# Kernel optimization log

Hardware: AMD Instinct MI355X
Metric: run time of the kernel (lower is better)

The kernel has to match this reference:

```python
import jax, jax.numpy as jnp
import numpy as np

ALPHA = 0.9
T = 809          # doc_len_limit hard-coded in fofe_tricontext_encoder
M = 16           # opt['max_len'] (cand_len_limit)
BN_EPS = 1e-5


def _cand_indices(T, M):
    # Enumeration order matches get_sample_index: outer over start s, inner over span.
    s_list, e_list = [], []
    for s in range(T):
        for span in range(min(M, T - s)):
            s_list.append(s)
            e_list.append(s + span)
    return np.asarray(s_list, np.int32), np.asarray(e_list, np.int32)

_S_IDX, _E_IDX = _cand_indices(T, M)          # [N_CANDS] = [12824]
_SPAN = (_E_IDX - _S_IDX).astype(np.int64)
# FOFE decay coefficient alpha^(e-s+1) for subtracting the prefix before the span
_COEF = (ALPHA ** (_SPAN + 1)).astype(np.float32)
# Lower-triangular FOFE prefix operator: A[t,k] = alpha^(t-k) for k<=t
_DIFF = np.subtract.outer(np.arange(T), np.arange(T))
_AFWD = np.where(_DIFF >= 0, ALPHA ** np.maximum(_DIFF, 0), 0.0).astype(np.float32)


def _bn(x, g, b, m, v):
    return (x - m) * jax.lax.rsqrt(v + BN_EPS) * g + b


def _forward(doc_emb, query_emb, W1, g1, b1, m1, v1, W2, g2, b2, m2, v2, W3):
    B, Tt, Dd = doc_emb.shape
    A = jnp.asarray(_AFWD)
    # forward FOFE prefixes F[t] = sum_{k<=t} alpha^(t-k) x[k]; inverse FOFE suffixes
    F = jnp.einsum('tk,bkd->btd', A, doc_emb)          # [B,T,Dd]
    R = jnp.einsum('tk,bkd->btd', A.T, doc_emb)        # [B,T,Dd]
    Fp = jnp.concatenate([jnp.zeros((B, 1, Dd), F.dtype), F], axis=1)   # Fp[:,s]=F[s-1]
    Rp = jnp.concatenate([R, jnp.zeros((B, 1, Dd), R.dtype)], axis=1)   # Rp[:,e+1]
    s_idx = jnp.asarray(_S_IDX)
    e_idx = jnp.asarray(_E_IDX)
    coef = jnp.asarray(_COEF)
    lctx = Fp[:, s_idx]                                 # left context excl cand
    cand = F[:, e_idx] - coef[None, :, None] * Fp[:, s_idx]  # FOFE of span [s,e]
    rctx = Rp[:, e_idx + 1]                             # right context excl cand
    doc_fofe = jnp.concatenate([lctx, cand, rctx], axis=-1)  # [B,N,3*Dd]
    # query FOFE (fofe_linear): z = sum_t alpha^(Lq-1-t) q[t]
    Lq = query_emb.shape[1]
    w = (ALPHA ** jnp.arange(Lq - 1, -1, -1, dtype=jnp.float32))
    qf = jnp.einsum('t,btd->bd', w, query_emb)          # [B,E]
    N = doc_fofe.shape[1]
    qf_b = jnp.broadcast_to(qf[:, None, :], (B, N, qf.shape[-1]))
    dq = jnp.concatenate([doc_fofe, qf_b], axis=-1)     # [B,N,3*Dd+E]
    x = dq.reshape(B * N, -1)
    h = jax.nn.relu(_bn(x @ W1.T, g1, b1, m1, v1))      # 1x1 conv == GEMM
    h = jax.nn.relu(_bn(h @ W2.T, g2, b2, m2, v2))
    out = (h @ W3.T).reshape(B, N, 2)                   # 2 class scores per candidate
    return out


def setup_inputs() -> dict:
    key = jax.random.key(0)
    ks = jax.random.split(key, 13)
    B, Lq, Dd, E = 4, 30, 304, 300
    Cin, H4, H2 = 3 * Dd + E, 1024, 512
    return {
        'doc_emb': jax.random.normal(ks[0], (B, T, Dd), jnp.float32),
        'query_emb': jax.random.normal(ks[1], (B, Lq, E), jnp.float32),
        'W1': jax.random.normal(ks[2], (H4, Cin), jnp.float32) / np.sqrt(Cin),
        'g1': jax.random.normal(ks[3], (H4,), jnp.float32),
        'b1': jax.random.normal(ks[4], (H4,), jnp.float32),
        'm1': jax.random.normal(ks[5], (H4,), jnp.float32),
        'v1': jax.random.uniform(ks[6], (H4,), jnp.float32),
        'W2': jax.random.normal(ks[7], (H2, H4), jnp.float32) / np.sqrt(H4),
        'g2': jax.random.normal(ks[8], (H2,), jnp.float32),
        'b2': jax.random.normal(ks[9], (H2,), jnp.float32),
        'm2': jax.random.normal(ks[10], (H2,), jnp.float32),
        'v2': jax.random.uniform(ks[11], (H2,), jnp.float32),
        'W3': jax.random.normal(ks[12], (2, H2), jnp.float32) / np.sqrt(H2),
    }


def reference(doc_emb, query_emb, W1, g1, b1, m1, v1, W2, g2, b2, m2, v2, W3):
    return _forward(doc_emb, query_emb, W1, g1, b1, m1, v1, W2, g2, b2, m2, v2, W3)
```

## Files before the change

kernel.cpp:

```cpp
#include <hip/hip_runtime.h>
#include <string.h>

#define T_LEN   809
#define DD      304
#define EE      300
#define LQ      30
#define NCAND   12824
#define NPAD    12928
#define CIN     1212
#define H1      1024
#define H2      512
#define BATCH   4
#define MROWS_F (BATCH * NPAD)
#define KS      320
#define TPAD    3328
#define NROWS_U 3240

#define MP_SCAN0   0
#define MP_W1      416
#define MP_W2      4256
#define MP_BIAS2   6304
#define MP_BASE    6306
#define MP_RMAP    7330
#define MP_TOTAL   7532

__device__ __constant__ float c_coef[16] = {
  0.9f, 0.81f, 0.729f, 0.6561f, 0.59049f, 0.531441f, 0.4782969f, 0.43046721f,
  0.387420489f, 0.3486784401f, 0.31381059609f, 0.282429536481f,
  0.2541865828329f, 0.22876792454961f, 0.205891132094649f, 0.1853020188851841f
};

__device__ __forceinline__ unsigned short f2bf(float f) {
  unsigned int u = __float_as_uint(f);
  u += 0x7fffu + ((u >> 16) & 1u);
  return (unsigned short)(u >> 16);
}
__device__ __forceinline__ float bf2f(unsigned int h) {
  return __uint_as_float(h << 16);
}

typedef const __attribute__((address_space(1))) unsigned int GU32;
typedef __attribute__((address_space(3))) unsigned int LU32;
__device__ __forceinline__ void async16(const unsigned short* g, unsigned short* l) {
  __builtin_amdgcn_global_load_lds((GU32*)g, (LU32*)l, 16, 0, 0);
}

__device__ __forceinline__ unsigned int comb2(unsigned int ul, unsigned int uc,
                                              unsigned int ue, float cf) {
  float xlo = bf2f(ul & 0xffff) + bf2f(ue & 0xffff) - cf * bf2f(uc & 0xffff);
  float xhi = bf2f(ul >> 16)    + bf2f(ue >> 16)    - cf * bf2f(uc >> 16);
  xlo = xlo > 0.f ? xlo : 0.f;
  xhi = xhi > 0.f ? xhi : 0.f;
  return (unsigned int)f2bf(xlo) | ((unsigned int)f2bf(xhi) << 16);
}
__device__ __forceinline__ unsigned int add2(unsigned int a, unsigned int b) {
  const float lo = bf2f(a & 0xffff) + bf2f(b & 0xffff);
  const float hi = bf2f(a >> 16)    + bf2f(b >> 16);
  return (unsigned int)f2bf(lo) | ((unsigned int)f2bf(hi) << 16);
}

__global__ __launch_bounds__(256) void k_prep(const float* __restrict__ doc,
                                              const float* __restrict__ qe,
                                              const float* __restrict__ W1,
                                              const float* __restrict__ g1,
                                              const float* __restrict__ b1,
                                              const float* __restrict__ m1,
                                              const float* __restrict__ v1,
                                              const float* __restrict__ W2,
                                              const float* __restrict__ g2,
                                              const float* __restrict__ b2,
                                              const float* __restrict__ m2,
                                              const float* __restrict__ v2,
                                              unsigned short* __restrict__ Fz,
                                              unsigned short* __restrict__ Rz,
                                              unsigned short* __restrict__ Wlc,
                                              unsigned short* __restrict__ Wr,
                                              unsigned short* __restrict__ W2b,
                                              float* __restrict__ bias2,
                                              float* __restrict__ baseW,
                                              unsigned int* __restrict__ rowmap)
{
  __shared__ float qs[EE];
  const int vb  = blockIdx.x;
  const int tid = threadIdx.x;

  if (vb < MP_W1) {
    const int dchunk = vb & 1;
    const int rest   = vb >> 1;
    const int tchunk = rest % 26;
    const int b      = (rest / 26) & 3;
    const int dir    = rest / 104;
    const int d  = dchunk * 256 + tid;
    const int t0 = tchunk * 32;
    if (dir == 0) {
      if (tchunk == 0 && d < KS) Fz[((size_t)b * 810) * KS + d] = 0;
      if (d >= DD) return;
      const float* db = doc + (size_t)b * T_LEN * DD + d;
      int start = t0 - 96; if (start < 0) start = 0;
      int end = t0 + 31; if (end > T_LEN - 1) end = T_LEN - 1;
      float s = 0.f;
      for (int t = start; t <= end; ++t) {
        s = fmaf(0.9f, s, db[(size_t)t * DD]);
        if (t >= t0) Fz[((size_t)b * 810 + 1 + t) * KS + d] = f2bf(s);
      }
    } else {
      if (tchunk == 0 && d < KS) Rz[((size_t)b * 810 + 809) * KS + d] = 0;
      if (d >= DD) return;
      const float* db = doc + (size_t)b * T_LEN * DD + d;
      int t1 = t0 + 31; if (t1 > T_LEN - 1) t1 = T_LEN - 1;
      int start = t1 + 96; if (start > T_LEN - 1) start = T_LEN - 1;
      float s = 0.f;
      for (int t = start; t >= t0; --t) {
        s = fmaf(0.9f, s, db[(size_t)t * DD]);
        if (t <= t1) Rz[((size_t)b * 810 + t) * KS + d] = f2bf(s);
      }
    }
  } else if (vb < MP_W2) {
    const int e = (vb - MP_W1) * 256 + tid;
    const int j = e / KS;
    const int k = e - j * KS;
    int jj, koff; unsigned short* dst; size_t idx;
    if (j < 1024)      { jj = j;        koff = k;       dst = Wlc; idx = (size_t)j * KS + k; }
    else if (j < 2048) { jj = j - 1024; koff = 304 + k; dst = Wlc; idx = (size_t)j * KS + k; }
    else               { jj = j - 2048; koff = 608 + k; dst = Wr;  idx = (size_t)(j - 2048) * KS + k; }
    float w = 0.f;
    if (k < 304) w = W1[(size_t)jj * CIN + koff] * g1[jj] * rsqrtf(v1[jj] + 1e-5f);
    dst[idx] = f2bf(w);
  } else if (vb < MP_BIAS2) {
    const int e = (vb - MP_W2) * 256 + tid;
    const int j = e >> 10;
    const int k = e & 1023;
    const float w = W2[(size_t)j * H1 + k] * g2[j] * rsqrtf(v2[j] + 1e-5f);
    W2b[(size_t)j * H1 + k] = f2bf(w);
  } else if (vb < MP_BASE) {
    const int i = (vb - MP_BIAS2) * 256 + tid;
    if (i < H2) {
      const float s = g2[i] * rsqrtf(v2[i] + 1e-5f);
      bias2[i] = b2[i] - m2[i] * s;
    }
  } else if (vb < MP_RMAP) {
    const int flat = vb - MP_BASE;
    const int b  = flat >> 8;
    const int jg = flat & 255;
    const float* q = qe + (size_t)b * LQ * EE;
    for (int k = tid; k < EE; k += 256) {
      float s = 0.f;
      for (int t = 0; t < LQ; ++t) s = fmaf(s, 0.9f, q[(size_t)t * EE + k]);
      qs[k] = s;
    }
    __syncthreads();
    const int wv   = tid >> 6;
    const int lane = tid & 63;
    const int j = jg * 4 + wv;
    const float* w = W1 + (size_t)j * CIN + 912;
    float acc = 0.f;
    for (int k = lane; k < EE; k += 64) acc = fmaf(qs[k], w[k], acc);
    #pragma unroll
    for (int off = 32; off; off >>= 1) acc += __shfl_down(acc, off);
    if (lane == 0) {
      const float sc = g1[j] * rsqrtf(v1[j] + 1e-5f);
      baseW[(size_t)b * 2048 + j]        = b1[j] - m1[j] * sc + acc * sc;
      baseW[(size_t)b * 2048 + 1024 + j] = 0.f;
    }
  } else {
    const int g = (vb - MP_RMAP) * 256 + tid;
    const int b  = g / NPAD;
    const int rr = g - b * NPAD;
    unsigned int mv = 0;
    if (rr < NCAND) {
      int s, span;
      if (rr < 12704) { s = rr >> 4; span = rr & 15; }
      else {
        const int x = rr - 12704;
        int d = 0;
        while (d < 14 && x >= (15 * (d + 1) - ((d + 1) * d) / 2)) ++d;
        span = x - (15 * d - (d * (d - 1)) / 2);
        s = 794 + d;
      }
      const unsigned int srow = (unsigned int)(b * 810 + s);
      const unsigned int erow = (unsigned int)(b * 810 + s + span + 1);
      mv = srow | (erow << 12) | ((unsigned int)span << 24);
    }
    rowmap[g] = mv;
  }
}

typedef __attribute__((ext_vector_type(8))) short frag8;
typedef __attribute__((ext_vector_type(4))) float f32x4;

#define GEMM_KLOOP(A_, B_, K_)                                                   \
  __shared__ __align__(16) unsigned short As[128 * 32];                          \
  __shared__ __align__(16) unsigned short Bs[128 * 32];                          \
  const int tid  = threadIdx.x;                                                  \
  const int lane = tid & 63;                                                     \
  const int wv   = tid >> 6;                                                     \
  const int wm   = wv & 1, wn = wv >> 1;                                         \
  const int lr = lane >> 2;                                                      \
  const int lc = lane & 3;                                                       \
  const int sc = lc ^ ((lr >> 1) & 3);                                           \
  const unsigned short* gA = A_ + ((size_t)bm * 128 + wv * 32 + lr) * K_ + sc * 8; \
  const unsigned short* gB = B_ + ((size_t)bn * 128 + wv * 32 + lr) * K_ + sc * 8; \
  const size_t row16 = (size_t)16 * K_;                                          \
  unsigned short* lA0 = &As[wv * 1024];                                          \
  unsigned short* lB0 = &Bs[wv * 1024];                                          \
  f32x4 acc[4][4];                                                               \
  _Pragma("unroll")                                                              \
  for (int i = 0; i < 4; ++i)                                                    \
    _Pragma("unroll")                                                            \
    for (int j = 0; j < 4; ++j) acc[i][j] = (f32x4){0.f, 0.f, 0.f, 0.f};         \
  const int arow = lane & 15;                                                    \
  const int pg   = (lane >> 4) ^ ((arow >> 1) & 3);                              \
  const int aoff = (wm * 64 + arow) * 32 + pg * 8;                               \
  const int boff = (wn * 64 + arow) * 32 + pg * 8;                               \
  for (int kc = 0; kc < K_; kc += 32) {                                          \
    __syncthreads();                                                             \
    async16(gA + kc,         lA0);                                               \
    async16(gA + kc + row16, lA0 + 512);                                         \
    async16(gB + kc,         lB0);                                               \
    async16(gB + kc + row16, lB0 + 512);                                         \
    __syncthreads();                                                             \
    frag8 a[4], b[4];                                                            \
    _Pragma("unroll")                                                            \
    for (int i = 0; i < 4; ++i) a[i] = *(const frag8*)&As[aoff + i * 512];       \
    _Pragma("unroll")                                                            \
    for (int i = 0; i < 4; ++i) b[i] = *(const frag8*)&Bs[boff + i * 512];       \
    _Pragma("unroll")                                                            \
    for (int i = 0; i < 4; ++i)                                                  \
      _Pragma("unroll")                                                          \
      for (int j = 0; j < 4; ++j)                                                \
        acc[i][j] = __builtin_amdgcn_mfma_f32_16x16x32_bf16(a[i], b[j], acc[i][j], 0, 0, 0); \
  }

__global__ __launch_bounds__(256, 4) void k_ugemm(const unsigned short* __restrict__ Fz,
                                                  const unsigned short* __restrict__ Wlc,
                                                  const unsigned short* __restrict__ Rz,
                                                  const unsigned short* __restrict__ Wr,
                                                  const float* __restrict__ baseW,
                                                  unsigned short* __restrict__ UF,
                                                  unsigned short* __restrict__ UR)
{
  int bx = blockIdx.x;
  const int isUF = (bx < 416);
  const unsigned short *Ap, *Bp; unsigned short* Cp; int bn, bm, Nout;
  if (isUF) { Ap = Fz; Bp = Wlc; Cp = UF; bn = bx & 15; bm = bx >> 4; Nout = 2048; }
  else { bx -= 416; Ap = Rz; Bp = Wr; Cp = UR; bn = bx & 7; bm = bx >> 3; Nout = 1024; }
  GEMM_KLOOP(Ap, Bp, KS)
  const int crow0 = bm * 128 + wm * 64 + ((lane >> 4) << 2);
  const int ccol0 = bn * 128 + wn * 64 + arow;
  #pragma unroll
  for (int i = 0; i < 4; ++i)
    #pragma unroll
    for (int j = 0; j < 4; ++j) {
      const int col = ccol0 + j * 16;
      #pragma unroll
      for (int r = 0; r < 4; ++r) {
        const int row = crow0 + i * 16 + r;
        float v = acc[i][j][r];
        if (isUF) {
          int bb = row / 810; if (bb > 3) bb = 3;
          v += baseW[(size_t)bb * 2048 + col];
        }
        Cp[(size_t)row * Nout + col] = f2bf(v);
      }
    }
}

__global__ __launch_bounds__(256) void k_ucr(const unsigned short* __restrict__ UF,
                                             const unsigned short* __restrict__ UR,
                                             unsigned short* __restrict__ UCR)
{
  const int c = blockIdx.x * 256 + threadIdx.x;
  if (c >= NROWS_U * 128) return;
  const int t  = c >> 7;
  const int kk = (c & 127) * 8;
  const uint4 a = *(const uint4*)(UF + (size_t)t * 2048 + 1024 + kk);
  const uint4 b = *(const uint4*)(UR + (size_t)t * 1024 + kk);
  uint4 o;
  o.x = add2(a.x, b.x);
  o.y = add2(a.y, b.y);
  o.z = add2(a.z, b.z);
  o.w = add2(a.w, b.w);
  *(uint4*)(UCR + (size_t)t * 1024 + kk) = o;
}

__global__ __launch_bounds__(512, 2) void k_gemm2f(const unsigned short* __restrict__ UF,
                                                   const unsigned short* __restrict__ UCR,
                                                   const unsigned short* __restrict__ W2b,
                                                   const unsigned int* __restrict__ rowmap,
                                                   const float* __restrict__ bias,
                                                   const float* __restrict__ W3,
                                                   float* __restrict__ out)
{
  __shared__ __align__(16) unsigned short As[128 * 32];
  __shared__ __align__(16) unsigned short Bs[512 * 32];

  const int orig = blockIdx.x;
  const int xcd = orig & 7, cidx = orig >> 3;
  const int bm = (xcd < 4 ? xcd * 51 : 204 + (xcd - 4) * 50) + cidx;

  const int tid  = threadIdx.x;
  const int lane = tid & 63;
  const int w    = tid >> 6;
  const int wm   = w & 1;
  const int wn   = w >> 1;
  const int arow = lane & 15;
  const int lr   = lane >> 2;
  const int lc   = lane & 3;
  const int sc   = lc ^ ((lr >> 1) & 3);

  const int rA    = tid >> 2;
  const int cA    = tid & 3;
  const int physA = cA ^ ((rA >> 1) & 3);
  const unsigned int mv = rowmap[bm * 128 + rA];
  const float cf = c_coef[mv >> 24];
  const unsigned short* pUL = UF  + (size_t)(mv & 4095) * 2048 + cA * 8;
  const unsigned short* pUE = UCR + (size_t)((mv >> 12) & 4095) * 1024 + cA * 8;
  unsigned short* wAd = &As[rA * 32 + physA * 8];

  const unsigned short* gB = W2b + ((size_t)(w * 64 + lr)) * H1 + sc * 8;
  unsigned short* lB = &Bs[w * 2048];

  const int pg   = (lane >> 4) ^ ((arow >> 1) & 3);
  const int aoff = (wm * 64 + arow) * 32 + pg * 8;
  const int boff = (wn * 128 + arow) * 32 + pg * 8;

  f32x4 acc[4][8];
  #pragma unroll
  for (int i = 0; i < 4; ++i)
    #pragma unroll
    for (int j = 0; j < 8; ++j) acc[i][j] = (f32x4){0.f, 0.f, 0.f, 0.f};

  uint4 vul = *(const uint4*)(pUL);
  uint4 vuc = *(const uint4*)(pUL + 1024);
  uint4 vue = *(const uint4*)(pUE);

  for (int kc = 0; kc < H1; kc += 32) {
    __syncthreads();
    async16(gB + kc,            lB);
    async16(gB + kc + 16 * H1,  lB + 512);
    async16(gB + kc + 32 * H1,  lB + 1024);
    async16(gB + kc + 48 * H1,  lB + 1536);
    {
      uint4 o;
      o.x = comb2(vul.x, vuc.x, vue.x, cf);
      o.y = comb2(vul.y, vuc.y, vue.y, cf);
      o.z = comb2(vul.z, vuc.z, vue.z, cf);
      o.w = comb2(vul.w, vuc.w, vue.w, cf);
      *(uint4*)wAd = o;
    }
    const int kn = kc + 32;
    if (kn < H1) {
      vul = *(const uint4*)(pUL + kn);
      vuc = *(const uint4*)(pUL + 1024 + kn);
      vue = *(const uint4*)(pUE + kn);
      __builtin_amdgcn_sched_barrier(0);
      asm volatile("s_waitcnt vmcnt(3) lgkmcnt(0)" ::: "memory");
    } else {
      __builtin_amdgcn_sched_barrier(0);
      asm volatile("s_waitcnt vmcnt(0) lgkmcnt(0)" ::: "memory");
    }
    __builtin_amdgcn_s_barrier();
    __builtin_amdgcn_sched_barrier(0);

    frag8 a[4], b[8];
    #pragma unroll
    for (int i = 0; i < 4; ++i) a[i] = *(const frag8*)&As[aoff + i * 512];
    #pragma unroll
    for (int j = 0; j < 8; ++j) b[j] = *(const frag8*)&Bs[boff + j * 512];
    #pragma unroll
    for (int i = 0; i < 4; ++i)
      #pragma unroll
      for (int j = 0; j < 8; ++j)
        acc[i][j] = __builtin_amdgcn_mfma_f32_16x16x32_bf16(a[i], b[j], acc[i][j], 0, 0, 0);
  }

  __syncthreads();
  float* redf = (float*)As;

  float bj[8], w0v[8], w1v[8];
  #pragma unroll
  for (int j = 0; j < 8; ++j) {
    const int col = wn * 128 + j * 16 + arow;
    bj[j]  = bias[col];
    w0v[j] = W3[col];
    w1v[j] = W3[H2 + col];
  }
  const int grp = lane >> 4;
  #pragma unroll
  for (int i = 0; i < 4; ++i)
    #pragma unroll
    for (int r = 0; r < 4; ++r) {
      float q0 = 0.f, q1 = 0.f;
      #pragma unroll
      for (int j = 0; j < 8; ++j) {
        float v = acc[i][j][r] + bj[j];
        v = v > 0.f ? v : 0.f;
        q0 = fmaf(v, w0v[j], q0);
        q1 = fmaf(v, w1v[j], q1);
      }
      #pragma unroll
      for (int m = 1; m < 16; m <<= 1) { q0 += __shfl_xor(q0, m); q1 += __shfl_xor(q1, m); }
      if (arow == 0) {
        const int rl = wm * 64 + i * 16 + grp * 4 + r;
        redf[rl * 8 + wn * 2 + 0] = q0;
        redf[rl * 8 + wn * 2 + 1] = q1;
      }
    }
  __syncthreads();
  if (tid < 256) {
    const int rl = tid >> 1, s = tid & 1;
    const float v = redf[rl * 8 + 0 + s] + redf[rl * 8 + 2 + s]
                  + redf[rl * 8 + 4 + s] + redf[rl * 8 + 6 + s];
    const int row = bm * 128 + rl;
    const int b   = row / NPAD;
    const int rr  = row - b * NPAD;
    if (rr < NCAND) out[((size_t)b * NCAND + rr) * 2 + s] = v;
  }
}

extern "C" void kernel_launch(void* const* d_in, const int* in_sizes, int n_in,
                              void* d_out, int out_size, void* d_ws, size_t ws_size,
                              hipStream_t stream)
{
  const float* doc = (const float*)d_in[0];
  const float* qe  = (const float*)d_in[1];
  const float* W1  = (const float*)d_in[2];
  const float* g1  = (const float*)d_in[3];
  const float* b1  = (const float*)d_in[4];
  const float* m1  = (const float*)d_in[5];
  const float* v1  = (const float*)d_in[6];
  const float* W2  = (const float*)d_in[7];
  const float* g2  = (const float*)d_in[8];
  const float* b2  = (const float*)d_in[9];
  const float* m2  = (const float*)d_in[10];
  const float* v2  = (const float*)d_in[11];
  const float* W3  = (const float*)d_in[12];
  float* out = (float*)d_out;

  char* ws = (char*)d_ws;
  size_t off = 0;
  auto alloc = [&](size_t bytes) -> void* {
    void* p = ws + off;
    off = (off + bytes + 255) & ~(size_t)255;
    return p;
  };
  unsigned short* Fz    = (unsigned short*)alloc((size_t)TPAD * KS * 2);
  unsigned short* Rz    = (unsigned short*)alloc((size_t)TPAD * KS * 2);
  unsigned short* Wlc   = (unsigned short*)alloc((size_t)2048 * KS * 2);
  unsigned short* Wr    = (unsigned short*)alloc((size_t)1024 * KS * 2);
  unsigned short* W2b   = (unsigned short*)alloc((size_t)H2 * H1 * 2);
  float*          bias2 = (float*)alloc((size_t)H2 * 4);
  float*          baseW = (float*)alloc((size_t)BATCH * 2048 * 4);
  unsigned short* UF    = (unsigned short*)alloc((size_t)TPAD * 2048 * 2);
  unsigned short* UR    = (unsigned short*)alloc((size_t)TPAD * 1024 * 2);
  unsigned short* UCR   = (unsigned short*)alloc((size_t)NROWS_U * 1024 * 2);
  unsigned int*   rowmap= (unsigned int*)alloc((size_t)MROWS_F * 4);
  (void)ws_size;

  k_prep<<<dim3(MP_TOTAL), 256, 0, stream>>>(doc, qe, W1, g1, b1, m1, v1,
                                             W2, g2, b2, m2, v2,
                                             Fz, Rz, Wlc, Wr, W2b, bias2, baseW, rowmap);
  k_ugemm<<<dim3(416 + 208), 256, 0, stream>>>(Fz, Wlc, Rz, Wr, baseW, UF, UR);
  k_ucr<<<dim3((NROWS_U * 128 + 255) / 256), 256, 0, stream>>>(UF, UR, UCR);
  k_gemm2f<<<dim3(404), 512, 0, stream>>>(UF, UCR, W2b, rowmap, bias2, W3, out);
}
```

Measured before the change: 240.9 us.

## Double-buffer LDS tiles in fused second GEMM and raise MFMA priority

Result: faster. 234.1 us (-2.8%).

```diff
diff --git a/kernel.cpp b/kernel.cpp
--- a/kernel.cpp
+++ b/kernel.cpp
@@ -291,8 +291,8 @@
                                                    const float* __restrict__ W3,
                                                    float* __restrict__ out)
 {
-  __shared__ __align__(16) unsigned short As[128 * 32];
-  __shared__ __align__(16) unsigned short Bs[512 * 32];
+  __shared__ __align__(16) unsigned short As[2 * 128 * 32];
+  __shared__ __align__(16) unsigned short Bs[2 * 512 * 32];
 
   const int orig = blockIdx.x;
   const int xcd = orig & 7, cidx = orig >> 3;
@@ -315,10 +315,8 @@
   const float cf = c_coef[mv >> 24];
   const unsigned short* pUL = UF  + (size_t)(mv & 4095) * 2048 + cA * 8;
   const unsigned short* pUE = UCR + (size_t)((mv >> 12) & 4095) * 1024 + cA * 8;
-  unsigned short* wAd = &As[rA * 32 + physA * 8];
 
   const unsigned short* gB = W2b + ((size_t)(w * 64 + lr)) * H1 + sc * 8;
-  unsigned short* lB = &Bs[w * 2048];
 
   const int pg   = (lane >> 4) ^ ((arow >> 1) & 3);
   const int aoff = (wm * 64 + arow) * 32 + pg * 8;
@@ -330,48 +328,74 @@
     #pragma unroll
     for (int j = 0; j < 8; ++j) acc[i][j] = (f32x4){0.f, 0.f, 0.f, 0.f};
 
-  uint4 vul = *(const uint4*)(pUL);
-  uint4 vuc = *(const uint4*)(pUL + 1024);
-  uint4 vue = *(const uint4*)(pUE);
-
-  for (int kc = 0; kc < H1; kc += 32) {
-    __syncthreads();
-    async16(gB + kc,            lB);
-    async16(gB + kc + 16 * H1,  lB + 512);
-    async16(gB + kc + 32 * H1,  lB + 1024);
-    async16(gB + kc + 48 * H1,  lB + 1536);
-    {
+  uint4 vulN = *(const uint4*)(pUL);
+  uint4 vucN = *(const uint4*)(pUL + 1024);
+  uint4 vueN = *(const uint4*)(pUE);
+  {
+    unsigned short* lB = &Bs[w * 2048];
+    async16(gB,           lB);
+    async16(gB + 16 * H1, lB + 512);
+    async16(gB + 32 * H1, lB + 1024);
+    async16(gB + 48 * H1, lB + 1536);
+  }
+  {
+    uint4 o;
+    o.x = comb2(vulN.x, vucN.x, vueN.x, cf);
+    o.y = comb2(vulN.y, vucN.y, vueN.y, cf);
+    o.z = comb2(vulN.z, vucN.z, vueN.z, cf);
+    o.w = comb2(vulN.w, vucN.w, vueN.w, cf);
+    *(uint4*)&As[rA * 32 + physA * 8] = o;
+  }
+  vulN = *(const uint4*)(pUL + 32);
+  vucN = *(const uint4*)(pUL + 1024 + 32);
+  vueN = *(const uint4*)(pUE + 32);
+  asm volatile("s_waitcnt lgkmcnt(0)" ::: "memory");
+  __builtin_amdgcn_sched_barrier(0);
+
+  for (int k = 0; k < 32; ++k) {
+    const int cur = k & 1, nxt = cur ^ 1;
+    __builtin_amdgcn_s_barrier();
+    __builtin_amdgcn_sched_barrier(0);
+    if (k < 31) {
+      const int kn = (k + 1) * 32;
+      unsigned short* lB = &Bs[nxt * 16384 + w * 2048];
+      async16(gB + kn,           lB);
+      async16(gB + kn + 16 * H1, lB + 512);
+      async16(gB + kn + 32 * H1, lB + 1024);
+      async16(gB + kn + 48 * H1, lB + 1536);
+      __builtin_amdgcn_sched_barrier(0);
+      asm volatile("s_waitcnt vmcnt(4)" ::: "memory");
+      __builtin_amdgcn_sched_barrier(0);
       uint4 o;
-      o.x = comb2(vul.x, vuc.x, vue.x, cf);
-      o.y = comb2(vul.y, vuc.y, vue.y, cf);
-      o.z = comb2(vul.z, vuc.z, vue.z, cf);
-      o.w = comb2(vul.w, vuc.w, vue.w, cf);
-      *(uint4*)wAd = o;
-    }
-    const int kn = kc + 32;
-    if (kn < H1) {
-      vul = *(const uint4*)(pUL + kn);
-      vuc = *(const uint4*)(pUL + 1024 + kn);
-      vue = *(const uint4*)(pUE + kn);
-      __builtin_amdgcn_sched_barrier(0);
-      asm volatile("s_waitcnt vmcnt(3) lgkmcnt(0)" ::: "memory");
+      o.x = comb2(vulN.x, vucN.x, vueN.x, cf);
+      o.y = comb2(vulN.y, vucN.y, vueN.y, cf);
+      o.z = comb2(vulN.z, vucN.z, vueN.z, cf);
+      o.w = comb2(vulN.w, vucN.w, vueN.w, cf);
+      *(uint4*)&As[nxt * 4096 + rA * 32 + physA * 8] = o;
+      if (k < 30) {
+        const int kg = (k + 2) * 32;
+        vulN = *(const uint4*)(pUL + kg);
+        vucN = *(const uint4*)(pUL + 1024 + kg);
+        vueN = *(const uint4*)(pUE + kg);
+      }
     } else {
       __builtin_amdgcn_sched_barrier(0);
-      asm volatile("s_waitcnt vmcnt(0) lgkmcnt(0)" ::: "memory");
-    }
-    __builtin_amdgcn_s_barrier();
+      asm volatile("s_waitcnt vmcnt(0)" ::: "memory");
+      __builtin_amdgcn_sched_barrier(0);
+    }
     __builtin_amdgcn_sched_barrier(0);
-
     frag8 a[4], b[8];
     #pragma unroll
-    for (int i = 0; i < 4; ++i) a[i] = *(const frag8*)&As[aoff + i * 512];
-    #pragma unroll
-    for (int j = 0; j < 8; ++j) b[j] = *(const frag8*)&Bs[boff + j * 512];
+    for (int i = 0; i < 4; ++i) a[i] = *(const frag8*)&As[cur * 4096 + aoff + i * 512];
+    #pragma unroll
+    for (int j = 0; j < 8; ++j) b[j] = *(const frag8*)&Bs[cur * 16384 + boff + j * 512];
+    __builtin_amdgcn_s_setprio(1);
     #pragma unroll
     for (int i = 0; i < 4; ++i)
       #pragma unroll
       for (int j = 0; j < 8; ++j)
         acc[i][j] = __builtin_amdgcn_mfma_f32_16x16x32_bf16(a[i], b[j], acc[i][j], 0, 0, 0);
+    __builtin_amdgcn_s_setprio(0);
   }
 
   __syncthreads();
```
